# Optimization experiments

Hardware: AMD Instinct MI355X
Metric: run time of the kernel (lower is better)

## Reference

```python
import jax, jax.numpy as jnp
import numpy as np

BSZ, SL, K, D_IN, D_OUT = 2, 1024, 24, 512, 512
K_U, K_Y = 3, 2
USE_HANKEL_L = False


def get_top_eigh(l, k, use_hankel_L):
    i = np.arange(1, l + 1, dtype=np.float64)
    s = i[:, None] + i[None, :]
    if use_hankel_L:
        Z = ((-1.0) ** (s - 2.0) + 1.0) * 8.0 / ((s + 3.0) * (s - 1.0) * (s + 1.0))
    else:
        Z = 2.0 / (s ** 3 - s)
    sigma, phi = np.linalg.eigh(Z)  # ascending
    return jnp.asarray(sigma[-k:], jnp.float32), jnp.asarray(phi[:, -k:], jnp.float32)


def shift(x, k):
    # causal shift along time axis 1, zero-padded at the front
    if k == 0:
        return x
    return jnp.pad(x, ((0, 0), (k, 0), (0, 0)))[:, : x.shape[1]]


def fft_causal_conv(filters, u):
    # filters: (l, k); u: (b, l, d) -> (b, l, k, d) causal convolution per filter
    l = u.shape[1]
    n = 2 * l
    F = jnp.fft.rfft(filters, n=n, axis=0)  # (n//2+1, k)
    U = jnp.fft.rfft(u, n=n, axis=1)        # (b, n//2+1, d)
    Y = jnp.fft.irfft(U[:, :, None, :] * F[None, :, :, None], n=n, axis=1)
    return Y[:, :l].astype(u.dtype)


def compute_ar_u(M_u, u):
    # ar_u[b,t,o] = sum_{i<k_u} M_u[i] @ u_{t-i}
    U = jnp.stack([shift(u, i) for i in range(M_u.shape[0])])  # (k_u, b, l, d_in)
    return jnp.einsum('koi,kbli->blo', M_u, U)


def compute_spectral(u, sigma, phi, M_phi_plus, M_phi_minus, m_y):
    l = u.shape[1]
    phi_s = phi * sigma ** 0.25  # eigenvalue-scaled spectral filters (l, k)
    U_plus = fft_causal_conv(phi_s, u)  # (b, l, k, d_in)
    spec = jnp.einsum('blki,koi->blo', U_plus, M_phi_plus)
    if not USE_HANKEL_L:
        # negative-featurization branch: filters modulated by (-1)^i
        alt = ((-1.0) ** jnp.arange(l)).astype(u.dtype)
        U_minus = fft_causal_conv(phi_s * alt[:, None], u)
        spec = spec + jnp.einsum('blki,koi->blo', U_minus, M_phi_minus)
    if m_y is not None:
        spec = shift(spec, m_y.shape[0])  # spectral features enter at lag k_y (paper: t-2)
    return spec


def compute_ar_y(m_y, y):
    # true short linear recurrence on outputs:
    # yhat_t = y_t + sum_{i=1}^{k_y} m_y[i-1] @ yhat_{t-i}; returns the correction term
    k_y, d_out = m_y.shape[0], m_y.shape[1]
    b = y.shape[0]

    def step(carry, y_t):  # carry: (k_y, b, d_out) = [yhat_{t-1}, ..., yhat_{t-k_y}]
        ar_t = jnp.einsum('koj,kbj->bo', m_y, carry)
        yhat_t = y_t + ar_t
        carry = jnp.concatenate([yhat_t[None], carry[:-1]], axis=0)
        return carry, ar_t

    y_tl = jnp.swapaxes(y, 0, 1)  # (l, b, d_out)
    _, ar = jax.lax.scan(step, jnp.zeros((k_y, b, d_out), y.dtype), y_tl)
    return jnp.swapaxes(ar, 0, 1)


def setup_inputs() -> dict:
    key = jax.random.key(0)
    k0, k1, k2, k3, k4 = jax.random.split(key, 5)
    inputs = jax.random.normal(k0, (BSZ, SL, D_IN), jnp.float32)
    M_u = jax.random.normal(k1, (K_U, D_OUT, D_IN), jnp.float32) * 0.02
    M_phi_plus = jax.random.normal(k2, (K, D_OUT, D_IN), jnp.float32) * 0.02
    M_phi_minus = jax.random.normal(k3, (K, D_OUT, D_IN), jnp.float32) * 0.02
    m_y = jax.random.normal(k4, (K_Y, D_OUT, D_OUT), jnp.float32) * 0.02
    sigma, phi = get_top_eigh(SL, K, USE_HANKEL_L)
    return {'inputs': inputs, 'M_u': M_u, 'M_phi_plus': M_phi_plus,
            'M_phi_minus': M_phi_minus, 'm_y': m_y, 'sigma': sigma, 'phi': phi}


def reference(inputs, M_u, M_phi_plus, M_phi_minus, m_y, sigma, phi):
    ar_u = compute_ar_u(M_u, inputs)
    spectral = compute_spectral(inputs, sigma, phi, M_phi_plus, M_phi_minus, m_y)
    y_t = ar_u + spectral
    y_t = y_t + compute_ar_y(m_y, y_t)  # learnable_m_y=True branch
    return y_t  # dropout p=0.0 (identity)
```

## Files before the change

### kernel.cpp

```cpp
#include <hip/hip_runtime.h>
#include <hip/hip_bf16.h>


typedef unsigned short u16;
typedef __attribute__((ext_vector_type(8))) short  vshort8;
typedef __attribute__((ext_vector_type(4))) short  vshort4;
typedef __attribute__((ext_vector_type(4))) float  f32x4;
typedef __attribute__((ext_vector_type(4))) unsigned int vuint4;

__device__ __forceinline__ u16 f2b(float x) {
  __hip_bfloat16 h = __float2bfloat16(x);
  return __builtin_bit_cast(u16, h);
}
__device__ __forceinline__ float b2f(u16 x) {
  unsigned int u = ((unsigned int)x) << 16;
  return __builtin_bit_cast(float, u);
}

__device__ __forceinline__ void gll16(const u16* g, u16* l) {
  __builtin_amdgcn_global_load_lds((__attribute__((address_space(1))) void*)g,
                                   (__attribute__((address_space(3))) void*)l,
                                   16, 0, 0);
}

#define A2T_B  25165824
#define A2T_CJ 3145728
#define A2T_KH 65536

struct GB {
  const u16* A; const u16* B;
  float* Cf; u16* Cb;
  const float* zf; float* out;
  u16* A2T; u16* Au;
  const u16* zp;
  u16* Pb; int cidx; int pthr;
  int M, N;
};

template<int V>
__global__ __launch_bounds__(V == 0 ? 512 : 256) void g2(GB a) {
  const int tid = threadIdx.x;
  int bn = blockIdx.x, bm = blockIdx.y;
  int zz = blockIdx.z;
  int cj = 0, cb = 0, cd = 0, slot = 0;
  int kbeg = 0, kend = 0;
  if (V == 0) {
    int f = blockIdx.x;
    int o = (f & 7) * 204 + (f >> 3);
    bm = o & 15; bn = o >> 4; kend = 512;
  }
  if (V == 1) {
    int f = blockIdx.x;
    int o = (f & 7) * 144 + (f >> 3);
    const int offs1[8] = {0, 256, 480, 672, 832, 960, 1056, 1120};
    cj = 0;
    if (o >= offs1[1]) cj = 1;
    if (o >= offs1[2]) cj = 2;
    if (o >= offs1[3]) cj = 3;
    if (o >= offs1[4]) cj = 4;
    if (o >= offs1[5]) cj = 5;
    if (o >= offs1[6]) cj = 6;
    if (o >= offs1[7]) cj = 7;
    int r = o - offs1[cj];
    int run = 8 - cj;
    int combo = r / run;
    bm = cj + (r - combo * run);
    int zzc = combo >> 2; bn = combo & 3;
    cb = zzc & 1; cd = bm - cj;
    slot = zzc * 8 + cj;
    kbeg = (zzc >> 1) * 1536; kend = kbeg + 1536;
  }
  if (V == 2) {
    int f = blockIdx.x;
    int o = (f & 7) * 68 + (f >> 3);
    const int offs2[16] = {0, 64, 124, 180, 232, 280, 324, 364,
                           400, 432, 460, 484, 504, 520, 532, 540};
    int s = 0;
#pragma unroll
    for (int c = 1; c < 16; ++c)
      if (o >= offs2[c]) s = c;
    int r = o - offs2[s];
    bm = s + (r >> 2); bn = r & 3;
    zz = s;
    kbeg = s * 1024; kend = kbeg + 1024;
  }
  const int m0 = bm * 128;
  const int n0 = (V == 0) ? bn * 256 : bn * 128;
  if (V == 3 || V == 5 || V == 6 || V == 7) kend = 1024;

  __shared__ u16 smem[V == 0 ? 24576 : 16384];
  f32x4 acc[4][4];
#pragma unroll
  for (int i = 0; i < 4; i++)
#pragma unroll
    for (int j = 0; j < 4; j++) acc[i][j] = f32x4{0.f, 0.f, 0.f, 0.f};

  const int lane = tid & 63, wv = tid >> 6;
  const int wr = (V == 0) ? (wv >> 2) : (wv >> 1);
  const int wc = (V == 0) ? (wv & 3) : (wv & 1);
  const u16* Ap = a.A;
  if (V == 5) Ap = a.A + (size_t)zz * 524288;
  const u16* zpl = a.zp + lane * 8;

  auto gaddrA = [&](int it, int k0) -> const u16* {
    int lrow = (it * 4 + wv) * 16 + (lane & 15);
    int kk = k0 + ((lane >> 4) << 3);
    if (V == 1) return Ap + (size_t)cd * 786432 + (size_t)lrow * 6144 + kk;
    if (V == 2) {
      int m = m0 + lrow, j = m >> 6, b = (m >> 5) & 1, c = m & 31;
      int tau = kk >> 9, p = kk & 511;
      if (tau > j) return zpl;
      return Ap + (size_t)(b * 1024 + c * 32 + j - tau) * 512 + p;
    }
    if (V == 3) { int m = m0 + lrow; return (m < a.M) ? Ap + (size_t)m * 1024 + kk : zpl; }
    if (V == 5) return Ap + (size_t)(m0 + lrow) * 1024 + kk;
    if (V == 6) return (lrow < 64) ? Ap + (size_t)lrow * 1024 + kk : zpl;
    if (lrow < 32) {
      int b = lrow & 1, k2 = lrow >> 1;
      return Ap + (size_t)(b * 32 + 2 * k2) * 1024 + kk;
    }
    return zpl;
  };
  auto gaddrB = [&](int it, int k0) -> const u16* {
    int lrow = (it * 4 + wv) * 16 + (lane & 15);
    int kk = k0 + ((lane >> 4) << 3);
    int n = n0 + lrow;
    if (V == 1) {
      int kh = kk >> 7, sp = kk & 127;
      return a.B + (size_t)cb * A2T_B + (size_t)cj * A2T_CJ
           + (size_t)kh * A2T_KH + (size_t)n * 128 + sp;
    }
    if (V == 2) {
      int tau = kk >> 9, p = kk & 511;
      return a.B + (size_t)tau * 524288 + (size_t)n * 1024 + p;
    }
    if (V == 3) {
      int jn = n >> 9, o = n & 511;
      return a.B + (size_t)(jn + 1) * 524288 + (size_t)o * 1024 + kk;
    }
    if (V == 5) {
      return (kk < 512)
          ? a.Pb + (size_t)a.cidx * 524288 + (size_t)n * 512 + kk
          : a.Pb + (size_t)(a.cidx - 1) * 524288 + (size_t)n * 512 + (kk - 512);
    }
    return (n < 512)
        ? a.B + (size_t)32 * 524288 + (size_t)n * 1024 + kk
        : a.B + (size_t)31 * 524288 + (size_t)(n - 512) * 1024 + kk;
  };

  auto stage = [&](int c, int k0) {
    if (V == 0) {
      int kk = k0 + ((lane >> 4) << 3);
      int lrowA = wv * 16 + (lane & 15);
      gll16(Ap + (size_t)(m0 + lrowA) * 512 + kk, smem + c * 4096 + wv * 512);
#pragma unroll
      for (int it = 0; it < 2; ++it) {
        int lrowB = (it * 8 + wv) * 16 + (lane & 15);
        gll16(a.B + (size_t)(n0 + lrowB) * 512 + kk,
              smem + 8192 + c * 8192 + (it * 8 + wv) * 512);
      }
    } else {
#pragma unroll
      for (int it = 0; it < 2; ++it) {
        int weff = wv + it * 4;
        gll16(gaddrA(it, k0), smem + c * 4096 + weff * 512);
        gll16(gaddrB(it, k0), smem + 8192 + c * 4096 + weff * 512);
      }
    }
  };

  if (kbeg < kend) stage(0, kbeg);
  __syncthreads();
  int cur = 0;
  for (int k0 = kbeg; k0 < kend; k0 += 32) {
    if (k0 + 32 < kend) stage(cur ^ 1, k0 + 32);
    vshort8 af[4], bf_[4];
#pragma unroll
    for (int s = 0; s < 4; s++) {
      af[s] = *(const vshort8*)&smem[cur * 4096 +
                (((wr * 4 + s) * 4 + (lane >> 4)) * 16 + (lane & 15)) * 8];
      if (V == 0)
        bf_[s] = *(const vshort8*)&smem[8192 + cur * 8192 +
                  (((wc * 4 + s) * 4 + (lane >> 4)) * 16 + (lane & 15)) * 8];
      else
        bf_[s] = *(const vshort8*)&smem[8192 + cur * 4096 +
                  (((wc * 4 + s) * 4 + (lane >> 4)) * 16 + (lane & 15)) * 8];
    }
#pragma unroll
    for (int i = 0; i < 4; i++)
#pragma unroll
      for (int j = 0; j < 4; j++)
        acc[i][j] = __builtin_amdgcn_mfma_f32_16x16x32_bf16(af[i], bf_[j], acc[i][j], 0, 0, 0);
    __syncthreads();
    cur ^= 1;
  }

  if (V == 0 && bn < 96) {
    const int strd = 136;
    const int b = m0 >> 10;
    const int cjw = (m0 & 1023) >> 7;
#pragma unroll
    for (int p = 0; p < 4; ++p) {
      __syncthreads();
      if (wc == p) {
#pragma unroll
        for (int i = 0; i < 4; i++) {
#pragma unroll
          for (int j = 0; j < 4; j++) {
            f32x4 v = acc[i][j];
            int mloc = wr * 64 + i * 16 + ((lane >> 4) << 2);
            int phys = j * 16 + (lane & 15);
            vshort4 pk = { (short)f2b(v[0]), (short)f2b(v[1]),
                           (short)f2b(v[2]), (short)f2b(v[3]) };
            *(vshort4*)&smem[phys * strd + mloc] = pk;
          }
        }
      }
      __syncthreads();
      int rowp = tid >> 3, t8 = tid & 7;
      int n = n0 + p * 64 + rowp;
      int o = n & 511, kh = n >> 9;
      u16* dst = a.A2T + (size_t)b * A2T_B + (size_t)cjw * A2T_CJ
               + (size_t)kh * A2T_KH + (size_t)o * 128 + t8 * 16;
      const u16* srcl = &smem[rowp * strd + t8 * 16];
      *(vuint4*)(dst)     = *(const vuint4*)(srcl);
      *(vuint4*)(dst + 8) = *(const vuint4*)(srcl + 8);
    }
    return;
  }

#pragma unroll
  for (int i = 0; i < 4; i++) {
    int em = m0 + wr * 64 + i * 16 + ((lane >> 4) << 2);
#pragma unroll
    for (int j = 0; j < 4; j++) {
      int n = n0 + wc * 64 + j * 16 + (lane & 15);
      f32x4 v = acc[i][j];
      if (V == 0) {
        int b = em >> 10, s = em & 1023;
        int jj = (n - 24576) >> 9, o = n & 511;
#pragma unroll
        for (int t = 0; t < 4; t++)
          a.Au[((size_t)(b * 3 + jj) * 1024 + (s + t)) * 512 + o] = f2b(v[t]);
      } else if (V == 1) {
        u16* C = a.Cb + (size_t)slot * 524288;
#pragma unroll
        for (int t = 0; t < 4; t++) C[(size_t)(em + t) * 512 + n] = f2b(v[t]);
      } else if (V == 2) {
        float* C = a.Cf + (size_t)zz * 1048576;
#pragma unroll
        for (int t = 0; t < 4; t++) C[(size_t)(em + t) * 512 + n] = v[t];
      } else if (V == 3) {
        int jj = n >> 9, oo = n & 511;
#pragma unroll
        for (int t = 0; t < 4; t++) {
          int m = em + t;
          if (m < a.M) {
            int b = m >> 5, c = m & 31;
            float zv = a.zf[(size_t)(jj * 64 + b * 32 + c) * 512 + oo];
            a.out[(size_t)b * 524288 + (size_t)(c * 32 + jj) * 512 + oo] = v[t] + zv;
          }
        }
      } else if (V == 5) {
        u16* C = a.Cb + (size_t)zz * 524288;
#pragma unroll
        for (int t = 0; t < 4; t++) C[(size_t)(em + t) * 1024 + n] = f2b(v[t]);
      } else if (V == 6) {
        int jrow = (n < 512) ? 31 : 30, oo = n & 511;
#pragma unroll
        for (int t = 0; t < 4; t++) {
          int m = em + t;
          if (m < 62) {
            int b = m & 1, c = m >> 1;
            a.Cf[(size_t)m * 1024 + n] =
                v[t] + a.zf[(size_t)(jrow * 64 + b * 32 + (c + 1)) * 512 + oo];
          }
        }
      } else {
        int jrow = (n < 512) ? 31 : 30, oo = n & 511;
#pragma unroll
        for (int t = 0; t < 4; t++) {
          int m = em + t;
          if (m < 32) {
            int b = m & 1, k2 = m >> 1;
            float val = v[t] + a.zf[(size_t)(jrow * 64 + b * 32 + 2 * k2) * 512 + oo];
            a.Cb[(size_t)(b * 32 + 2 * k2 + 1) * 1024 + n] = f2b(val);
          }
        }
      }
    }
  }

  if (V == 5) {
    if (zz >= a.pthr) {
      const int strd = 136;
      u16* Pout = a.Pb + (size_t)(a.cidx + 1 + zz) * 524288;
#pragma unroll
      for (int p = 0; p < 2; ++p) {
        __syncthreads();
        if (wc == p) {
#pragma unroll
          for (int i = 0; i < 4; i++) {
#pragma unroll
            for (int j = 0; j < 4; j++) {
              f32x4 v = acc[i][j];
              int mloc = wr * 64 + i * 16 + ((lane >> 4) << 2);
              int phys = j * 16 + (lane & 15);
              vshort4 pk = { (short)f2b(v[0]), (short)f2b(v[1]),
                             (short)f2b(v[2]), (short)f2b(v[3]) };
              *(vshort4*)&smem[phys * strd + mloc] = pk;
            }
          }
        }
        __syncthreads();
        int rowp = tid >> 2, t4 = tid & 3;
        u16* dst = Pout + (size_t)(n0 + p * 64 + rowp) * 512 + m0 + t4 * 32;
        const u16* srcl = &smem[rowp * strd + t4 * 32];
#pragma unroll
        for (int q = 0; q < 4; ++q)
          *(vuint4*)(dst + q * 8) = *(const vuint4*)(srcl + q * 8);
      }
    }
  }
}

__global__ void k_prep_phis(const float* __restrict__ phi, const float* __restrict__ sigma,
                            float* __restrict__ phis) {
  int i = blockIdx.x * 256 + threadIdx.x;
  if (i >= 1024 * 48) return;
  int tau = i / 48, kf = i % 48, k = (kf >= 24) ? kf - 24 : kf;
  float v = phi[tau * 24 + k] * powf(sigma[k], 0.25f);
  if (kf >= 24 && (tau & 1)) v = -v;
  phis[i] = v;
}

__global__ void k_prep_all(const float* __restrict__ u, const float* __restrict__ Mp,
                           const float* __restrict__ Mm, const float* __restrict__ Mu,
                           const float* __restrict__ phis,
                           u16* __restrict__ X, u16* __restrict__ W1,
                           u16* __restrict__ Wtoep) {
  int gid = blockIdx.x * 256 + threadIdx.x;
  if (gid < 262144) {
    int i4 = gid * 4;
    f32x4 v = *(const f32x4*)(u + i4);
    vshort4 pk = { (short)f2b(v[0]), (short)f2b(v[1]), (short)f2b(v[2]), (short)f2b(v[3]) };
    *(vshort4*)(X + i4) = pk;
  }
#pragma unroll
  for (int r = 0; r < 4; ++r) {
    int item = gid + r * 1048576;
    if (item < 3342336) {
      int i4 = item * 4;
      const float* src; int off;
      if (i4 < 6291456) { src = Mp; off = i4; }
      else if (i4 < 12582912) { src = Mm; off = i4 - 6291456; }
      else { src = Mu; off = i4 - 12582912; }
      f32x4 v = *(const f32x4*)(src + off);
      vshort4 pk = { (short)f2b(v[0]), (short)f2b(v[1]), (short)f2b(v[2]), (short)f2b(v[3]) };
      *(vshort4*)(W1 + i4) = pk;
    }
  }
  if (gid < 786432) {
    int i = gid * 8;
    int kap = i % 6144, row = i / 6144;
    int tp = row & 127, d = row >> 7;
    int kh = kap >> 7, sp = kap & 127;
    int tau0 = d * 128 + tp - sp;
    u16 vals[8];
#pragma unroll
    for (int e = 0; e < 8; ++e) {
      int tau = tau0 - e;
      vals[e] = (tau >= 0 && tau < 1024) ? f2b(phis[tau * 48 + kh]) : (u16)0;
    }
    *(vuint4*)(Wtoep + i) = *(const vuint4*)vals;
  }
}

__global__ void k_initTop(const float* __restrict__ my, u16* __restrict__ Top,
                          u16* __restrict__ P) {
  int i = blockIdx.x * 256 + threadIdx.x;
  if (i >= 2097152) return;
  if (i < 1048576) {
    int mat = i >> 19, rem = i & 524287, o = rem >> 10, k = rem & 1023;
    u16 v;
    if (mat == 0) v = (k == o) ? (u16)0x3F80 : (u16)0;
    else v = (k < 512) ? f2b(my[o * 512 + k]) : f2b(my[262144 + o * 512 + (k - 512)]);
    Top[i] = v;
  } else {
    int j = i - 1048576;
    int mat = j >> 19, rem = j & 524287, n = rem >> 9, m = rem & 511;
    u16 v;
    if (mat == 0) v = (n == m) ? (u16)0x3F80 : (u16)0;
    else v = (n < 512) ? f2b(my[m * 512 + n]) : f2b(my[262144 + m * 512 + (n - 512)]);
    P[(size_t)mat * 524288 + (size_t)n * 512 + m] = v;
  }
}

__device__ __forceinline__ void addp(float* acc, vuint4 v) {
  const unsigned int* vu = (const unsigned int*)&v;
#pragma unroll
  for (int e = 0; e < 4; ++e) {
    unsigned int pw = vu[e];
    acc[2 * e]     += __builtin_bit_cast(float, (pw & 0xffffu) << 16);
    acc[2 * e + 1] += __builtin_bit_cast(float, pw & 0xffff0000u);
  }
}

__global__ void k_combine(const u16* __restrict__ parts, const u16* __restrict__ Au,
                          u16* __restrict__ ybf) {
  int i = blockIdx.x * 256 + threadIdx.x;
  if (i >= 131072) return;
  int og = i & 63, t = (i >> 6) & 1023, b = i >> 16;
  float acc[8];
#pragma unroll
  for (int e = 0; e < 8; ++e) acc[e] = 0.f;
#pragma unroll
  for (int j = 0; j < 3; j++)
    if (t >= j)
      addp(acc, *(const vuint4*)(Au + ((size_t)(b * 3 + j) * 1024 + (t - j)) * 512 + og * 8));
  if (t >= 2) {
    int tp = t - 2, bmv = tp >> 7;
#pragma unroll
    for (int g = 0; g < 8; ++g) {
      if ((g & 1) != b) continue;
      const u16* base = parts + (size_t)(g * 8) * 524288 + (size_t)tp * 512 + og * 8;
      for (int j = 0; j <= bmv; ++j)
        addp(acc, *(const vuint4*)(base + (size_t)j * 524288));
    }
  }
  u16 o16[8];
#pragma unroll
  for (int e = 0; e < 8; ++e) o16[e] = f2b(acc[e]);
  *(vuint4*)(ybf + ((size_t)(b * 1024 + t)) * 512 + og * 8) = *(vuint4*)o16;
}

__global__ void k_zred(const float* __restrict__ zp, float* __restrict__ z,
                       u16* __restrict__ Wm, float* __restrict__ bnd,
                       u16* __restrict__ Abnd) {
  int i = blockIdx.x * 256 + threadIdx.x;
  if (i < 2048) bnd[i] = 0.f;
  if (i < 1024) { Abnd[i] = 0; Abnd[32768 + i] = 0; }
  if (i >= 1048576) return;
  int nsum = (i >> 16) + 1;
  float s = 0.f;
  for (int j = 0; j < nsum; ++j) s += zp[(size_t)j * 1048576 + i];
  z[i] = s;
  int m = i >> 9, jj = m >> 6, rem = m & 63, b = rem >> 5, c = rem & 31, oo = i & 511;
  if (jj == 31) Wm[(size_t)((c << 1) | b) * 1024 + oo] = f2b(s);
  if (jj == 30) Wm[(size_t)((c << 1) | b) * 1024 + 512 + oo] = f2b(s);
}

__global__ __launch_bounds__(256) void k_bnd2(const u16* __restrict__ Top,
                                              const float* __restrict__ ubuf,
                                              float* __restrict__ bnd,
                                              u16* __restrict__ Abnd, int k) {
  __shared__ float st[2048];
  int tid = threadIdx.x;
  const float* s0 = bnd + (size_t)k * 2048;
  for (int j = tid; j < 2048; j += 256) st[j] = s0[j];
  __syncthreads();
  int q4 = blockIdx.x * 256 + tid;
  int q = q4 >> 2, quarter = q4 & 3;
  int b = q >> 10, kk = q & 1023;
  const u16* row = (kk < 512) ? Top + (size_t)34 * 524288 + (size_t)kk * 1024
                              : Top + (size_t)33 * 524288 + (size_t)(kk - 512) * 1024;
  const float* stb = st + b * 1024 + quarter * 256;
  const u16* rp = row + quarter * 256;
  float sum = 0.f;
  for (int t = 0; t < 32; ++t) {
    vuint4 v = *(const vuint4*)(rp + t * 8);
    const unsigned int* vu = (const unsigned int*)&v;
#pragma unroll
    for (int e = 0; e < 4; ++e) {
      unsigned int pw = vu[e];
      float lo = __builtin_bit_cast(float, (pw & 0xffffu) << 16);
      float hi = __builtin_bit_cast(float, pw & 0xffff0000u);
      sum += lo * stb[t * 8 + e * 2] + hi * stb[t * 8 + e * 2 + 1];
    }
  }
  sum += __shfl_xor(sum, 1);
  sum += __shfl_xor(sum, 2);
  if (quarter == 0) {
    float s = sum + ubuf[(size_t)(4 * k + b) * 1024 + kk];
    bnd[(size_t)(k + 1) * 2048 + b * 1024 + kk] = s;
    Abnd[(size_t)(b * 32 + 2 * k + 2) * 1024 + kk] = f2b(s);
  }
}

extern "C" void kernel_launch(void* const* d_in, const int* in_sizes, int n_in,
                              void* d_out, int out_size, void* d_ws, size_t ws_size,
                              hipStream_t stream) {
  const float* u     = (const float*)d_in[0];
  const float* Mu    = (const float*)d_in[1];
  const float* Mp    = (const float*)d_in[2];
  const float* Mm    = (const float*)d_in[3];
  const float* my    = (const float*)d_in[4];
  const float* sigma = (const float*)d_in[5];
  const float* phi   = (const float*)d_in[6];
  float* out = (float*)d_out;

  char* ws = (char*)d_ws;
  size_t off = 0;
  auto alc = [&](size_t b) { size_t p = off; off = (off + b + 255) & ~(size_t)255; return p; };
  u16*  X     = (u16*)(ws + alc(2097152));
  u16*  Wtoep = (u16*)(ws + alc(12582912));
  u16*  A2T   = (u16*)(ws + alc(100663296));
  u16*  Au    = (u16*)(ws + alc(6291456));
  u16*  W1    = (u16*)(ws + alc(26738688));
  char* ptail = ws + alc(40370176); (void)ptail;
  float* phis = (float*)(ws + alc(196608));
  float* bnd  = (float*)(ws + alc(131072));
  u16*  Abnd  = (u16*)(ws + alc(131072));
  u16*  Wm    = (u16*)(ws + alc(131072));
  float* ubuf = (float*)(ws + alc(262144));
  u16*  zpad  = (u16*)(ws + alc(32768));
  if (off > ws_size) return;
  u16*  partsBf = (u16*)W1;
  float* zparts = (float*)W1;
  u16*  ybf = A2T;
  float* zf = (float*)((char*)A2T + (4 << 20));
  u16*  Top = (u16*)((char*)A2T + (size_t)(8 << 20));
  u16*  P   = (u16*)((char*)A2T + (size_t)(44 << 20));

  hipMemsetAsync(zpad, 0, 32768, stream);

  k_prep_phis<<<dim3(192), 256, 0, stream>>>(phi, sigma, phis);
  k_prep_all<<<dim3(4096), 256, 0, stream>>>(u, Mp, Mm, Mu, phis, X, W1, Wtoep);

  {
    GB g{}; g.A = X; g.B = W1; g.A2T = A2T; g.Au = Au; g.zp = zpad;
    g.M = 2048; g.N = 26112;
    g2<0><<<dim3(1632), 512, 0, stream>>>(g);
  }
  {
    GB g{}; g.A = Wtoep; g.B = A2T; g.Cb = partsBf; g.zp = zpad;
    g.M = 1024; g.N = 512;
    g2<1><<<dim3(1152), 256, 0, stream>>>(g);
  }
  k_combine<<<dim3(512), 256, 0, stream>>>(partsBf, Au, ybf);

  k_initTop<<<dim3(8192), 256, 0, stream>>>(my, Top, P);
  {
    const int cs[5] = {1, 2, 4, 8, 16};
    for (int li = 0; li < 5; ++li) {
      int c = cs[li];
      GB s{}; s.A = Top + 524288; s.Cb = Top + (size_t)(c + 1) * 524288;
      s.Pb = P; s.cidx = c; s.pthr = c - 2;
      s.zp = zpad; s.M = 512; s.N = 1024;
      g2<5><<<dim3(8, 4, c), 256, 0, stream>>>(s);
    }
    GB s{}; s.A = Top + (size_t)31 * 524288;
    s.Cb = Top + (size_t)33 * 524288;
    s.Pb = P; s.cidx = 32; s.pthr = 99;
    s.zp = zpad; s.M = 512; s.N = 1024;
    g2<5><<<dim3(8, 4, 2), 256, 0, stream>>>(s);
  }

  {
    GB g{}; g.A = ybf; g.B = Top; g.Cf = zparts; g.zp = zpad;
    g.M = 2048; g.N = 512;
    g2<2><<<dim3(544), 256, 0, stream>>>(g);
  }
  k_zred<<<dim3(4096), 256, 0, stream>>>(zparts, zf, Wm, bnd, Abnd);

  {
    GB g{}; g.A = Wm; g.B = Top; g.Cf = ubuf; g.zf = zf; g.zp = zpad;
    g.M = 64; g.N = 1024;
    g2<6><<<dim3(8, 1, 1), 256, 0, stream>>>(g);
  }
  for (int k = 0; k < 15; ++k)
    k_bnd2<<<dim3(32), 256, 0, stream>>>(Top, ubuf, bnd, Abnd, k);
  {
    GB g{}; g.A = Abnd; g.B = Top; g.Cb = Abnd; g.zf = zf; g.zp = zpad;
    g.M = 32; g.N = 1024;
    g2<7><<<dim3(8, 1, 1), 256, 0, stream>>>(g);
  }

  {
    GB g{}; g.A = Abnd; g.B = Top; g.zf = zf; g.out = out; g.zp = zpad;
    g.M = 64; g.N = 16384;
    g2<3><<<dim3(128, 1, 1), 256, 0, stream>>>(g);
  }
}
```

Measured before the change: 692.9 us.

## Double recurrence stride to four blocks, halving sequential boundary steps

Measured after the change: 710.8 us. 1.03x slower.

```diff
diff --git a/kernel.cpp b/kernel.cpp
--- a/kernel.cpp
+++ b/kernel.cpp
@@ -86,7 +86,7 @@
   }
   const int m0 = bm * 128;
   const int n0 = (V == 0) ? bn * 256 : bn * 128;
-  if (V == 3 || V == 5 || V == 6 || V == 7) kend = 1024;
+  if (V == 3 || V == 5 || V == 6 || V == 7 || V == 8 || V == 9) kend = 1024;
 
   __shared__ u16 smem[V == 0 ? 24576 : 16384];
   f32x4 acc[4][4];
@@ -115,9 +115,23 @@
     if (V == 3) { int m = m0 + lrow; return (m < a.M) ? Ap + (size_t)m * 1024 + kk : zpl; }
     if (V == 5) return Ap + (size_t)(m0 + lrow) * 1024 + kk;
     if (V == 6) return (lrow < 64) ? Ap + (size_t)lrow * 1024 + kk : zpl;
-    if (lrow < 32) {
-      int b = lrow & 1, k2 = lrow >> 1;
-      return Ap + (size_t)(b * 32 + 2 * k2) * 1024 + kk;
+    if (V == 7) {
+      if (lrow < 32) {
+        int b = lrow & 1, k2 = lrow >> 1;
+        return Ap + (size_t)(b * 32 + 2 * k2) * 1024 + kk;
+      }
+      return zpl;
+    }
+    if (V == 8) {
+      if (lrow < 14) {
+        int b = lrow & 1, k = lrow >> 1;
+        return Ap + (size_t)((8 * k) | b) * 1024 + kk;
+      }
+      return zpl;
+    }
+    if (lrow < 16) {
+      int b = lrow & 1, k = lrow >> 1;
+      return Ap + (size_t)(b * 32 + 4 * k) * 1024 + kk;
     }
     return zpl;
   };
@@ -142,6 +156,11 @@
       return (kk < 512)
           ? a.Pb + (size_t)a.cidx * 524288 + (size_t)n * 512 + kk
           : a.Pb + (size_t)(a.cidx - 1) * 524288 + (size_t)n * 512 + (kk - 512);
+    }
+    if (V == 8 || V == 9) {
+      return (n < 512)
+          ? a.B + (size_t)34 * 524288 + (size_t)n * 1024 + kk
+          : a.B + (size_t)33 * 524288 + (size_t)(n - 512) * 1024 + kk;
     }
     return (n < 512)
         ? a.B + (size_t)32 * 524288 + (size_t)n * 1024 + kk
@@ -272,11 +291,12 @@
           int m = em + t;
           if (m < 62) {
             int b = m & 1, c = m >> 1;
-            a.Cf[(size_t)m * 1024 + n] =
-                v[t] + a.zf[(size_t)(jrow * 64 + b * 32 + (c + 1)) * 512 + oo];
+            float val = v[t] + a.zf[(size_t)(jrow * 64 + b * 32 + (c + 1)) * 512 + oo];
+            a.Cf[(size_t)m * 1024 + n] = val;
+            a.Cb[(size_t)m * 1024 + n] = f2b(val);
           }
         }
-      } else {
+      } else if (V == 7) {
         int jrow = (n < 512) ? 31 : 30, oo = n & 511;
 #pragma unroll
         for (int t = 0; t < 4; t++) {
@@ -285,6 +305,26 @@
             int b = m & 1, k2 = m >> 1;
             float val = v[t] + a.zf[(size_t)(jrow * 64 + b * 32 + 2 * k2) * 512 + oo];
             a.Cb[(size_t)(b * 32 + 2 * k2 + 1) * 1024 + n] = f2b(val);
+          }
+        }
+      } else if (V == 8) {
+#pragma unroll
+        for (int t = 0; t < 4; t++) {
+          int m = em + t;
+          if (m < 14) {
+            int b = m & 1, k = m >> 1;
+            a.Cf[(size_t)m * 1024 + n] =
+                v[t] + a.zf[(size_t)((8 * k + 4) | b) * 1024 + n];
+          }
+        }
+      } else {
+#pragma unroll
+        for (int t = 0; t < 4; t++) {
+          int m = em + t;
+          if (m < 16) {
+            int b = m & 1, k = m >> 1;
+            float val = v[t] + a.zf[(size_t)((8 * k) | b) * 1024 + n];
+            a.Cb[(size_t)(b * 32 + 4 * k + 2) * 1024 + n] = f2b(val);
           }
         }
       }
@@ -450,8 +490,8 @@
   if (jj == 30) Wm[(size_t)((c << 1) | b) * 1024 + 512 + oo] = f2b(s);
 }
 
-__global__ __launch_bounds__(256) void k_bnd2(const u16* __restrict__ Top,
-                                              const float* __restrict__ ubuf,
+__global__ __launch_bounds__(256) void k_bnd4(const u16* __restrict__ Top,
+                                              const float* __restrict__ ubuf2,
                                               float* __restrict__ bnd,
                                               u16* __restrict__ Abnd, int k) {
   __shared__ float st[2048];
@@ -462,8 +502,8 @@
   int q4 = blockIdx.x * 256 + tid;
   int q = q4 >> 2, quarter = q4 & 3;
   int b = q >> 10, kk = q & 1023;
-  const u16* row = (kk < 512) ? Top + (size_t)34 * 524288 + (size_t)kk * 1024
-                              : Top + (size_t)33 * 524288 + (size_t)(kk - 512) * 1024;
+  const u16* row = (kk < 512) ? Top + (size_t)36 * 524288 + (size_t)kk * 1024
+                              : Top + (size_t)35 * 524288 + (size_t)(kk - 512) * 1024;
   const float* stb = st + b * 1024 + quarter * 256;
   const u16* rp = row + quarter * 256;
   float sum = 0.f;
@@ -481,9 +521,9 @@
   sum += __shfl_xor(sum, 1);
   sum += __shfl_xor(sum, 2);
   if (quarter == 0) {
-    float s = sum + ubuf[(size_t)(4 * k + b) * 1024 + kk];
+    float s = sum + ubuf2[(size_t)((k << 1) | b) * 1024 + kk];
     bnd[(size_t)(k + 1) * 2048 + b * 1024 + kk] = s;
-    Abnd[(size_t)(b * 32 + 2 * k + 2) * 1024 + kk] = f2b(s);
+    Abnd[(size_t)(b * 32 + 4 * k + 4) * 1024 + kk] = f2b(s);
   }
 }
 
@@ -513,6 +553,8 @@
   u16*  Abnd  = (u16*)(ws + alc(131072));
   u16*  Wm    = (u16*)(ws + alc(131072));
   float* ubuf = (float*)(ws + alc(262144));
+  u16*  Ubf   = (u16*)(ws + alc(131072));
+  float* ubuf2 = (float*)(ws + alc(65536));
   u16*  zpad  = (u16*)(ws + alc(32768));
   if (off > ws_size) return;
   u16*  partsBf = (u16*)W1;
@@ -520,7 +562,7 @@
   u16*  ybf = A2T;
   float* zf = (float*)((char*)A2T + (4 << 20));
   u16*  Top = (u16*)((char*)A2T + (size_t)(8 << 20));
-  u16*  P   = (u16*)((char*)A2T + (size_t)(44 << 20));
+  u16*  P   = (u16*)((char*)A2T + (size_t)(46 << 20));
 
   hipMemsetAsync(zpad, 0, 32768, stream);
 
@@ -551,9 +593,14 @@
     }
     GB s{}; s.A = Top + (size_t)31 * 524288;
     s.Cb = Top + (size_t)33 * 524288;
-    s.Pb = P; s.cidx = 32; s.pthr = 99;
+    s.Pb = P; s.cidx = 32; s.pthr = 0;
     s.zp = zpad; s.M = 512; s.N = 1024;
     g2<5><<<dim3(8, 4, 2), 256, 0, stream>>>(s);
+    GB t{}; t.A = Top + (size_t)33 * 524288;
+    t.Cb = Top + (size_t)35 * 524288;
+    t.Pb = P; t.cidx = 34; t.pthr = 99;
+    t.zp = zpad; t.M = 512; t.N = 1024;
+    g2<5><<<dim3(8, 4, 2), 256, 0, stream>>>(t);
   }
 
   {
@@ -564,12 +611,22 @@
   k_zred<<<dim3(4096), 256, 0, stream>>>(zparts, zf, Wm, bnd, Abnd);
 
   {
-    GB g{}; g.A = Wm; g.B = Top; g.Cf = ubuf; g.zf = zf; g.zp = zpad;
+    GB g{}; g.A = Wm; g.B = Top; g.Cf = ubuf; g.Cb = Ubf; g.zf = zf; g.zp = zpad;
     g.M = 64; g.N = 1024;
     g2<6><<<dim3(8, 1, 1), 256, 0, stream>>>(g);
   }
-  for (int k = 0; k < 15; ++k)
-    k_bnd2<<<dim3(32), 256, 0, stream>>>(Top, ubuf, bnd, Abnd, k);
+  {
+    GB g{}; g.A = Ubf; g.B = Top; g.Cf = ubuf2; g.zf = ubuf; g.zp = zpad;
+    g.M = 16; g.N = 1024;
+    g2<8><<<dim3(8, 1, 1), 256, 0, stream>>>(g);
+  }
+  for (int k = 0; k < 7; ++k)
+    k_bnd4<<<dim3(32), 256, 0, stream>>>(Top, ubuf2, bnd, Abnd, k);
+  {
+    GB g{}; g.A = Abnd; g.B = Top; g.Cb = Abnd; g.zf = ubuf; g.zp = zpad;
+    g.M = 16; g.N = 1024;
+    g2<9><<<dim3(8, 1, 1), 256, 0, stream>>>(g);
+  }
   {
     GB g{}; g.A = Abnd; g.B = Top; g.Cb = Abnd; g.zf = zf; g.zp = zpad;
     g.M = 32; g.N = 1024;
```
